# Kernel tuning notes

Hardware: AMD Instinct MI355X
Metric: run time of the kernel (lower is better)

The kernel has to match this reference:

```python
import jax, jax.numpy as jnp
import numpy as np

EPS = 1e-06

def _pairwise_giou(pred, target):
    # pred: [B,P,4], target: [B,G,4] -> gious [B,P,G]
    p = pred[:, :, None, :]   # [B,P,1,4]
    t = target[:, None, :, :] # [B,1,G,4]
    pw = jnp.clip(p[..., 2] - p[..., 0] + 1.0, 0.0)
    ph = jnp.clip(p[..., 3] - p[..., 1] + 1.0, 0.0)
    tw = jnp.clip(t[..., 2] - t[..., 0] + 1.0, 0.0)
    th = jnp.clip(t[..., 3] - t[..., 1] + 1.0, 0.0)
    pred_areas = pw * ph
    target_areas = tw * th
    ix1 = jnp.maximum(p[..., 0], t[..., 0])
    iy1 = jnp.maximum(p[..., 1], t[..., 1])
    ix2 = jnp.minimum(p[..., 2], t[..., 2])
    iy2 = jnp.minimum(p[..., 3], t[..., 3])
    iw = jnp.clip(ix2 - ix1 + 1.0, 0.0)
    ih = jnp.clip(iy2 - iy1 + 1.0, 0.0)
    inter = iw * ih
    unions = pred_areas + target_areas - inter
    ious = jnp.maximum(inter / unions, EPS)
    ox1 = jnp.minimum(p[..., 0], t[..., 0])
    oy1 = jnp.minimum(p[..., 1], t[..., 1])
    ox2 = jnp.maximum(p[..., 2], t[..., 2])
    oy2 = jnp.maximum(p[..., 3], t[..., 3])
    ow = jnp.clip(ox2 - ox1 + 1.0, 0.0)
    oh = jnp.clip(oy2 - oy1 + 1.0, 0.0)
    outer = ow * oh
    gious = ious - (outer - unions) / outer
    return jnp.clip(gious, -1.0, 1.0)


def setup_inputs() -> dict:
    key = jax.random.key(0)
    k1, k2, k3, k4, k5 = jax.random.split(key, 5)
    B, P, G = 32, 2048, 512
    IMG = 1024.0
    # gt boxes: [B,G,4] with x1<=x2, y1<=y2
    gxy = jax.random.uniform(k1, (B, G, 2), dtype=jnp.float32) * (IMG - 64.0)
    gwh = jax.random.uniform(k2, (B, G, 2), dtype=jnp.float32) * 64.0 + 1.0
    imgs_box = jnp.concatenate([gxy, gxy + gwh], axis=-1)
    # pred boxes: [B,P,4]
    pxy = jax.random.uniform(k3, (B, P, 2), dtype=jnp.float32) * (IMG - 64.0)
    pwh = jax.random.uniform(k4, (B, P, 2), dtype=jnp.float32) * 64.0 + 1.0
    pre_BOX = jnp.concatenate([pxy, pxy + pwh], axis=-1)
    labels = jax.random.randint(k5, (B,), 0, 10, dtype=jnp.int64 if jax.config.jax_enable_x64 else jnp.int32)
    return {"imgs_box": imgs_box, "pre_BOX": pre_BOX, "labels": labels}


def reference(imgs_box, pre_BOX, labels):
    B = labels.shape[0]
    gious = _pairwise_giou(pre_BOX, imgs_box)      # [B,P,G]
    max_giou = jnp.max(gious, axis=-1)             # [B,P]
    batch_loss = jnp.sum(1.0 - max_giou)
    return batch_loss / B
```

## Files before the change

### kernel.cpp

```cpp
#include <hip/hip_runtime.h>


__global__ __launch_bounds__(512) void giou_partial_kernel(
    const float4* __restrict__ tgt,
    const float4* __restrict__ pred,
    float* __restrict__ partial,
    int P, int G)
{
    __shared__ float4 sT[512];
    __shared__ float  sA[512];
    __shared__ float  sM[1024];

    const int b    = blockIdx.y;
    const int tid  = threadIdx.x;
    const int lane = tid & 63;
    const int wid  = tid >> 6;

    for (int g = tid; g < G; g += 512) {
        float4 t = tgt[b * G + g];
        t.z += 1.0f; t.w += 1.0f;
        sT[g] = t;
        sA[g] = (t.z - t.x) * (t.w - t.y);
    }
    __syncthreads();

    const int p0 = blockIdx.x * 128 + lane;
    const int p1 = p0 + 64;
    float4 pb0 = pred[b * P + min(p0, P - 1)];
    float4 pb1 = pred[b * P + min(p1, P - 1)];
    pb0.z += 1.0f; pb0.w += 1.0f;
    pb1.z += 1.0f; pb1.w += 1.0f;
    const float pa0 = (pb0.z - pb0.x) * (pb0.w - pb0.y);
    const float pa1 = (pb1.z - pb1.x) * (pb1.w - pb1.y);

    const int gq = (G + 7) >> 3;
    const int g0 = wid * gq;
    const int g1 = min(g0 + gq, G);

    float m0 = 0.0f, m1 = 0.0f;

    #pragma unroll 4
    for (int g = g0; g < g1; ++g) {
        const float4 t  = sT[g];
        const float  ta = sA[g];

        {
            float iw = fmaxf(fminf(pb0.z, t.z) - fmaxf(pb0.x, t.x), 0.0f);
            float ih = fmaxf(fminf(pb0.w, t.w) - fmaxf(pb0.y, t.y), 0.0f);
            float inter = iw * ih;
            float un  = (pa0 + ta) - inter;
            float iou = inter * __builtin_amdgcn_rcpf(un);
            float ow  = fmaxf(pb0.z, t.z) - fminf(pb0.x, t.x);
            float oh  = fmaxf(pb0.w, t.w) - fminf(pb0.y, t.y);
            float gi  = __builtin_fmaf(un, __builtin_amdgcn_rcpf(ow * oh), iou);
            m0 = fmaxf(m0, gi);
        }
        {
            float iw = fmaxf(fminf(pb1.z, t.z) - fmaxf(pb1.x, t.x), 0.0f);
            float ih = fmaxf(fminf(pb1.w, t.w) - fmaxf(pb1.y, t.y), 0.0f);
            float inter = iw * ih;
            float un  = (pa1 + ta) - inter;
            float iou = inter * __builtin_amdgcn_rcpf(un);
            float ow  = fmaxf(pb1.z, t.z) - fminf(pb1.x, t.x);
            float oh  = fmaxf(pb1.w, t.w) - fminf(pb1.y, t.y);
            float gi  = __builtin_fmaf(un, __builtin_amdgcn_rcpf(ow * oh), iou);
            m1 = fmaxf(m1, gi);
        }
    }

    sM[tid]       = m0;
    sM[512 + tid] = m1;
    __syncthreads();

    if (wid == 0) {
        float mm0 = sM[lane];
        float mm1 = sM[512 + lane];
        #pragma unroll
        for (int w = 1; w < 8; ++w) {
            mm0 = fmaxf(mm0, sM[w * 64 + lane]);
            mm1 = fmaxf(mm1, sM[512 + w * 64 + lane]);
        }
        float v = ((p0 < P) ? (2.0f - mm0) : 0.0f)
                + ((p1 < P) ? (2.0f - mm1) : 0.0f);
        #pragma unroll
        for (int off = 32; off > 0; off >>= 1)
            v += __shfl_down(v, off, 64);
        if (lane == 0)
            partial[blockIdx.y * gridDim.x + blockIdx.x] = v;
    }
}

__global__ __launch_bounds__(256) void giou_reduce_kernel(
    const float* __restrict__ partial, float* __restrict__ out, int n, float invB)
{
    const int tid = threadIdx.x;
    float v = 0.0f;
    for (int i = tid; i < n; i += 256) v += partial[i];

    #pragma unroll
    for (int off = 32; off > 0; off >>= 1)
        v += __shfl_down(v, off, 64);

    __shared__ float sW[4];
    const int wid = tid >> 6;
    if ((tid & 63) == 0) sW[wid] = v;
    __syncthreads();
    if (tid == 0)
        out[0] = (sW[0] + sW[1] + sW[2] + sW[3]) * invB;
}

extern "C" void kernel_launch(void* const* d_in, const int* in_sizes, int n_in,
                              void* d_out, int out_size, void* d_ws, size_t ws_size,
                              hipStream_t stream) {
    const float* imgs_box = (const float*)d_in[0];
    const float* pre_box  = (const float*)d_in[1];

    const int B = in_sizes[2];
    const int G = in_sizes[0] / (4 * B);
    const int P = in_sizes[1] / (4 * B);

    float* partial = (float*)d_ws;

    const int pblocks = (P + 127) / 128;
    dim3 grid(pblocks, B);
    giou_partial_kernel<<<grid, 512, 0, stream>>>(
        (const float4*)imgs_box, (const float4*)pre_box, partial, P, G);

    const int n = pblocks * B;
    giou_reduce_kernel<<<1, 256, 0, stream>>>(partial, (float*)d_out, n, 1.0f / (float)B);
}
```

Baseline: 30.77 us.

## Merge GIoU divisions into one reciprocal, widen per-thread tiles, and fuse reduction with atomics

The GIoU expression is rewritten so each pair needs one reciprocal instead of two, and the outer box size is derived algebraically from the intersection extents. Each thread now handles four pred boxes, with 1024-thread blocks and 16 waves splitting G. Targets are loaded into shared memory in chunks so G can exceed 512. The separate reduce kernel is replaced by a memset plus a per-block atomicAdd. The changes aim to cut transcendental and ALU work and one kernel launch, at the cost of more register pressure, fewer blocks, and a non-deterministic float summation order.

```diff
diff --git a/kernel.cpp b/kernel.cpp
--- a/kernel.cpp
+++ b/kernel.cpp
@@ -1,112 +1,96 @@
 #include <hip/hip_runtime.h>
 
 
-__global__ __launch_bounds__(512) void giou_partial_kernel(
+constexpr int NP   = 4;
+constexpr int GMAX = 512;
+
+__global__ __launch_bounds__(1024) void giou_kernel(
     const float4* __restrict__ tgt,
     const float4* __restrict__ pred,
-    float* __restrict__ partial,
-    int P, int G)
+    float* __restrict__ out,
+    int P, int G, float invB)
 {
-    __shared__ float4 sT[512];
-    __shared__ float  sA[512];
-    __shared__ float  sM[1024];
+    __shared__ float4 sT[GMAX];
+    __shared__ float  sA[GMAX];
+    __shared__ float  sM[NP][1024];
 
     const int b    = blockIdx.y;
     const int tid  = threadIdx.x;
     const int lane = tid & 63;
     const int wid  = tid >> 6;
 
-    for (int g = tid; g < G; g += 512) {
-        float4 t = tgt[b * G + g];
-        t.z += 1.0f; t.w += 1.0f;
-        sT[g] = t;
-        sA[g] = (t.z - t.x) * (t.w - t.y);
+    float4 pb[NP]; float pa[NP], pw[NP], ph[NP];
+    const int pbase = blockIdx.x * (NP * 64) + lane;
+    #pragma unroll
+    for (int k = 0; k < NP; ++k) {
+        float4 v = pred[b * P + min(pbase + 64 * k, P - 1)];
+        v.z += 1.0f; v.w += 1.0f;
+        pb[k] = v;
+        pw[k] = v.z - v.x;
+        ph[k] = v.w - v.y;
+        pa[k] = pw[k] * ph[k];
     }
-    __syncthreads();
 
-    const int p0 = blockIdx.x * 128 + lane;
-    const int p1 = p0 + 64;
-    float4 pb0 = pred[b * P + min(p0, P - 1)];
-    float4 pb1 = pred[b * P + min(p1, P - 1)];
-    pb0.z += 1.0f; pb0.w += 1.0f;
-    pb1.z += 1.0f; pb1.w += 1.0f;
-    const float pa0 = (pb0.z - pb0.x) * (pb0.w - pb0.y);
-    const float pa1 = (pb1.z - pb1.x) * (pb1.w - pb1.y);
+    float m[NP];
+    #pragma unroll
+    for (int k = 0; k < NP; ++k) m[k] = 0.0f;
 
-    const int gq = (G + 7) >> 3;
-    const int g0 = wid * gq;
-    const int g1 = min(g0 + gq, G);
+    for (int gb = 0; gb < G; gb += GMAX) {
+        const int gcnt = min(GMAX, G - gb);
+        __syncthreads();
+        for (int g = tid; g < gcnt; g += 1024) {
+            float4 t = tgt[b * G + gb + g];
+            t.z += 1.0f; t.w += 1.0f;
+            sT[g] = t;
+            sA[g] = (t.z - t.x) * (t.w - t.y);
+        }
+        __syncthreads();
 
-    float m0 = 0.0f, m1 = 0.0f;
+        const int gq = (gcnt + 15) >> 4;
+        const int g0 = wid * gq;
+        const int g1 = min(g0 + gq, gcnt);
 
-    #pragma unroll 4
-    for (int g = g0; g < g1; ++g) {
-        const float4 t  = sT[g];
-        const float  ta = sA[g];
-
-        {
-            float iw = fmaxf(fminf(pb0.z, t.z) - fmaxf(pb0.x, t.x), 0.0f);
-            float ih = fmaxf(fminf(pb0.w, t.w) - fmaxf(pb0.y, t.y), 0.0f);
-            float inter = iw * ih;
-            float un  = (pa0 + ta) - inter;
-            float iou = inter * __builtin_amdgcn_rcpf(un);
-            float ow  = fmaxf(pb0.z, t.z) - fminf(pb0.x, t.x);
-            float oh  = fmaxf(pb0.w, t.w) - fminf(pb0.y, t.y);
-            float gi  = __builtin_fmaf(un, __builtin_amdgcn_rcpf(ow * oh), iou);
-            m0 = fmaxf(m0, gi);
-        }
-        {
-            float iw = fmaxf(fminf(pb1.z, t.z) - fmaxf(pb1.x, t.x), 0.0f);
-            float ih = fmaxf(fminf(pb1.w, t.w) - fmaxf(pb1.y, t.y), 0.0f);
-            float inter = iw * ih;
-            float un  = (pa1 + ta) - inter;
-            float iou = inter * __builtin_amdgcn_rcpf(un);
-            float ow  = fmaxf(pb1.z, t.z) - fminf(pb1.x, t.x);
-            float oh  = fmaxf(pb1.w, t.w) - fminf(pb1.y, t.y);
-            float gi  = __builtin_fmaf(un, __builtin_amdgcn_rcpf(ow * oh), iou);
-            m1 = fmaxf(m1, gi);
+        #pragma unroll 2
+        for (int g = g0; g < g1; ++g) {
+            const float4 t  = sT[g];
+            const float  ta = sA[g];
+            const float  tw = t.z - t.x;
+            const float  th = t.w - t.y;
+            #pragma unroll
+            for (int k = 0; k < NP; ++k) {
+                float iwr = fminf(pb[k].z, t.z) - fmaxf(pb[k].x, t.x);
+                float ihr = fminf(pb[k].w, t.w) - fmaxf(pb[k].y, t.y);
+                float inter = fmaxf(iwr, 0.0f) * fmaxf(ihr, 0.0f);
+                float ow  = (pw[k] + tw) - iwr;
+                float oh  = (ph[k] + th) - ihr;
+                float outer = ow * oh;
+                float un  = (pa[k] + ta) - inter;
+                float num = __builtin_fmaf(un, un, inter * outer);
+                float gi  = num * __builtin_amdgcn_rcpf(un * outer);
+                m[k] = fmaxf(m[k], gi);
+            }
         }
     }
 
-    sM[tid]       = m0;
-    sM[512 + tid] = m1;
+    #pragma unroll
+    for (int k = 0; k < NP; ++k) sM[k][tid] = m[k];
     __syncthreads();
 
     if (wid == 0) {
-        float mm0 = sM[lane];
-        float mm1 = sM[512 + lane];
+        float v = 0.0f;
         #pragma unroll
-        for (int w = 1; w < 8; ++w) {
-            mm0 = fmaxf(mm0, sM[w * 64 + lane]);
-            mm1 = fmaxf(mm1, sM[512 + w * 64 + lane]);
+        for (int k = 0; k < NP; ++k) {
+            float mm = sM[k][lane];
+            #pragma unroll
+            for (int w = 1; w < 16; ++w) mm = fmaxf(mm, sM[k][w * 64 + lane]);
+            v += (pbase + 64 * k < P) ? (2.0f - mm) : 0.0f;
         }
-        float v = ((p0 < P) ? (2.0f - mm0) : 0.0f)
-                + ((p1 < P) ? (2.0f - mm1) : 0.0f);
         #pragma unroll
         for (int off = 32; off > 0; off >>= 1)
             v += __shfl_down(v, off, 64);
         if (lane == 0)
-            partial[blockIdx.y * gridDim.x + blockIdx.x] = v;
+            atomicAdd(out, v * invB);
     }
-}
-
-__global__ __launch_bounds__(256) void giou_reduce_kernel(
-    const float* __restrict__ partial, float* __restrict__ out, int n, float invB)
-{
-    const int tid = threadIdx.x;
-    float v = 0.0f;
-    for (int i = tid; i < n; i += 256) v += partial[i];
-
-    #pragma unroll
-    for (int off = 32; off > 0; off >>= 1)
-        v += __shfl_down(v, off, 64);
-
-    __shared__ float sW[4];
-    const int wid = tid >> 6;
-    if ((tid & 63) == 0) sW[wid] = v;
-    __syncthreads();
-    if (tid == 0)
-        out[0] = (sW[0] + sW[1] + sW[2] + sW[3]) * invB;
 }
 
 extern "C" void kernel_launch(void* const* d_in, const int* in_sizes, int n_in,
@@ -119,13 +103,11 @@
     const int G = in_sizes[0] / (4 * B);
     const int P = in_sizes[1] / (4 * B);
 
-    float* partial = (float*)d_ws;
+    hipMemsetAsync(d_out, 0, sizeof(float), stream);
 
-    const int pblocks = (P + 127) / 128;
+    const int pblocks = (P + NP * 64 - 1) / (NP * 64);
     dim3 grid(pblocks, B);
-    giou_partial_kernel<<<grid, 512, 0, stream>>>(
-        (const float4*)imgs_box, (const float4*)pre_box, partial, P, G);
-
-    const int n = pblocks * B;
-    giou_reduce_kernel<<<1, 256, 0, stream>>>(partial, (float*)d_out, n, 1.0f / (float)B);
+    giou_kernel<<<grid, 1024, 0, stream>>>(
+        (const float4*)imgs_box, (const float4*)pre_box, (float*)d_out,
+        P, G, 1.0f / (float)B);
 }
```

New measurement: 33.31 us. 1.08x slower.
